# Kernel tuning notes

Measured on AMD Instinct MI355X. Metric: run time of the kernel, lower is better.

The kernel has to match this reference:

```python
import jax, jax.numpy as jnp
import numpy as np

DIM = 256      # channel dim
NW = 7         # n_win per side
HEADS = 8
TOPK = 4
KVW = 4        # kv_per_win (ada_avgpool output side)
EPS = 1e-6


def _dwconv(x, w, b):
    # depthwise conv, NHWC, 'SAME' == padding k//2 for odd kernels
    y = jax.lax.conv_general_dilated(
        x, w, (1, 1), 'SAME',
        dimension_numbers=('NHWC', 'HWIO', 'NHWC'),
        feature_group_count=x.shape[-1])
    return y + b


def _ln(x, g, b):
    mu = x.mean(-1, keepdims=True)
    var = ((x - mu) ** 2).mean(-1, keepdims=True)
    return (x - mu) * jax.lax.rsqrt(var + EPS) * g + b


def _bra(x, qkv_w, qkv_b, wo_w, wo_b, lepe_w, lepe_b):
    # BiLevelRoutingAttention, x: (n, H, W, C)
    n, H, W, C = x.shape
    hw, ww = H // NW, W // NW          # window size (8, 8)
    scale = C ** -0.5                   # qk_dim ** -0.5 (BiFormer uses full qk_dim)
    qkv = x @ qkv_w.T + qkv_b           # (n, H, W, 3C)
    # window partition: n (j hw) (i ww) c -> n (j i) hw ww c
    qkv_win = qkv.reshape(n, NW, hw, NW, ww, 3 * C)
    qkv_win = qkv_win.transpose(0, 1, 3, 2, 4, 5).reshape(n, NW * NW, hw, ww, 3 * C)
    q = qkv_win[..., :C]                # (n, p2, hw, ww, C)
    kv = qkv_win[..., C:]               # (n, p2, hw, ww, 2C)
    # --- window-level routing (q/k detached in torch; no fwd effect) ---
    q_win = q.mean((2, 3))              # (n, p2, C)
    k_win = kv[..., :C].mean((2, 3))    # (n, p2, C)
    logits = jnp.einsum('npc,nqc->npq', q_win * scale, k_win)
    _, idx = jax.lax.top_k(logits, TOPK)            # (n, p2, k)
    # --- kv downsample: adaptive avg pool (hw,ww)->(KVW,KVW), exact 2x2 mean here ---
    fh, fw = hw // KVW, ww // KVW
    kv_pix = kv.reshape(n, NW * NW, KVW, fh, KVW, fw, 2 * C).mean((3, 5))
    kv_pix = kv_pix.reshape(n, NW * NW, KVW * KVW, 2 * C)   # (n, p2, w2, 2C)
    # --- gather top-k windows' kv ---
    kv_sel = jax.vmap(lambda t, ix: t[ix])(kv_pix, idx)     # (n, p2, k, w2, 2C)
    cph = C // HEADS
    k_sel = kv_sel[..., :C].reshape(n, NW * NW, TOPK * KVW * KVW, HEADS, cph)
    v_sel = kv_sel[..., C:].reshape(n, NW * NW, TOPK * KVW * KVW, HEADS, cph)
    q_pix = q.reshape(n, NW * NW, hw * ww, HEADS, cph)
    # --- windowed attention over gathered tokens ---
    att = jnp.einsum('npqmc,npsmc->npmqs', q_pix * scale, k_sel)
    att = jax.nn.softmax(att, axis=-1)
    out = jnp.einsum('npmqs,npsmc->npqmc', att, v_sel)
    out = out.reshape(n, NW, NW, hw, ww, C).transpose(0, 1, 3, 2, 4, 5).reshape(n, H, W, C)
    # --- lepe: depthwise 5x5 on v over the full image ---
    v_img = qkv[..., 2 * C:]
    out = out + _dwconv(v_img, lepe_w, lepe_b)
    return out @ wo_w.T + wo_b


def setup_inputs() -> dict:
    key = jax.random.key(0)
    ks = jax.random.split(key, 8)
    C, s = DIM, 0.02
    p = {}
    p['x'] = jax.random.normal(ks[0], (16, C, 56, 56), jnp.float32)
    p['pos_w'] = jax.random.normal(ks[1], (3, 3, 1, C), jnp.float32) * s
    p['pos_b'] = jnp.zeros((C,), jnp.float32)
    p['ln1_g'] = jnp.ones((C,), jnp.float32)
    p['ln1_b'] = jnp.zeros((C,), jnp.float32)
    p['ln2_g'] = jnp.ones((C,), jnp.float32)
    p['ln2_b'] = jnp.zeros((C,), jnp.float32)
    p['qkv_w'] = jax.random.normal(ks[2], (3 * C, C), jnp.float32) * s
    p['qkv_b'] = jnp.zeros((3 * C,), jnp.float32)
    p['wo_w'] = jax.random.normal(ks[3], (C, C), jnp.float32) * s
    p['wo_b'] = jnp.zeros((C,), jnp.float32)
    p['lepe_w'] = jax.random.normal(ks[4], (5, 5, 1, C), jnp.float32) * s
    p['lepe_b'] = jnp.zeros((C,), jnp.float32)
    p['fc1_w'] = jax.random.normal(ks[5], (4 * C, C), jnp.float32) * s
    p['fc1_b'] = jnp.zeros((4 * C,), jnp.float32)
    p['fc2_w'] = jax.random.normal(ks[6], (C, 4 * C), jnp.float32) * s
    p['fc2_b'] = jnp.zeros((C,), jnp.float32)
    return p


def reference(x, pos_w, pos_b, ln1_g, ln1_b, ln2_g, ln2_b, qkv_w, qkv_b,
              wo_w, wo_b, lepe_w, lepe_b, fc1_w, fc1_b, fc2_w, fc2_b):
    xh = x.transpose(0, 2, 3, 1)                       # NCHW -> NHWC
    xh = xh + _dwconv(xh, pos_w, pos_b)                # pos embed (dw 3x3)
    xh = xh + _bra(_ln(xh, ln1_g, ln1_b), qkv_w, qkv_b, wo_w, wo_b, lepe_w, lepe_b)
    h = _ln(xh, ln2_g, ln2_b)
    h = jax.nn.gelu(h @ fc1_w.T + fc1_b, approximate=False)
    xh = xh + (h @ fc2_w.T + fc2_b)
    return xh.transpose(0, 3, 1, 2)                    # NHWC -> NCHW
```

## Files before the change

kernel.cpp:

```cpp
#include <hip/hip_runtime.h>
#include <math.h>

static constexpr int NIMG = 16;
static constexpr int TOK  = NIMG * 56 * 56;
static constexpr size_t TC = (size_t)TOK * 256;
static constexpr int PTOK = 784 * 16;

typedef __bf16 bf16x8 __attribute__((ext_vector_type(8)));
typedef float  f32x4  __attribute__((ext_vector_type(4)));

__device__ inline float bf2f(unsigned short u) {
  unsigned int i = ((unsigned int)u) << 16; float f; __builtin_memcpy(&f, &i, 4); return f;
}
__device__ inline unsigned short f2bf(float f) {
  unsigned int i; __builtin_memcpy(&i, &f, 4);
  unsigned int r = i + 0x7fffu + ((i >> 16) & 1u);
  return (unsigned short)(r >> 16);
}

__global__ __launch_bounds__(256) void nchw2nhwc(const float* __restrict__ x,
                                                 float* __restrict__ y) {
  __shared__ float T[32][37];
  int nh = blockIdx.z;
  int n = nh / 56, h = nh % 56;
  int c0 = blockIdx.y * 32, w0 = blockIdx.x * 32;
  int tid = threadIdx.x;
  int wlim = 56 - w0; if (wlim > 32) wlim = 32;
  {
    int ci = tid >> 3, w = (tid & 7) * 4;
    if (w < wlim) {
      f32x4 v = *(const f32x4*)&x[(((size_t)n * 256 + c0 + ci) * 56 + h) * 56 + w0 + w];
#pragma unroll
      for (int j = 0; j < 4; j++) T[ci][w + j] = v[j];
    }
  }
  __syncthreads();
  {
    int wi = tid >> 3, cq = tid & 7;
    if (wi < wlim) {
      f32x4 o;
#pragma unroll
      for (int k = 0; k < 4; k++) o[k] = T[cq * 4 + k][wi];
      *(f32x4*)&y[(((size_t)n * 56 + h) * 56 + w0 + wi) * 256 + c0 + cq * 4] = o;
    }
  }
}

__global__ __launch_bounds__(256) void nhwc2nchw(const float* __restrict__ y,
                                                 float* __restrict__ o) {
  __shared__ float T[32][37];
  int nh = blockIdx.z;
  int n = nh / 56, h = nh % 56;
  int w0 = blockIdx.x * 32, c0 = blockIdx.y * 32;
  int tid = threadIdx.x;
  int wlim = 56 - w0; if (wlim > 32) wlim = 32;
  {
    int wi = tid >> 3, cq = tid & 7;
    if (wi < wlim) {
      f32x4 v = *(const f32x4*)&y[(((size_t)n * 56 + h) * 56 + w0 + wi) * 256 + c0 + cq * 4];
#pragma unroll
      for (int k = 0; k < 4; k++) T[wi][cq * 4 + k] = v[k];
    }
  }
  __syncthreads();
  {
    int ci = tid >> 3, w = (tid & 7) * 4;
    if (w < wlim) {
      f32x4 ov;
#pragma unroll
      for (int j = 0; j < 4; j++) ov[j] = T[w + j][ci];
      *(f32x4*)&o[(((size_t)n * 256 + c0 + ci) * 56 + h) * 56 + w0 + w] = ov;
    }
  }
}

__global__ __launch_bounds__(256) void posconv_kernel(const float* __restrict__ xt,
                                                      const float* __restrict__ w,
                                                      const float* __restrict__ b,
                                                      float* __restrict__ xh) {
  int bid = blockIdx.x;
  int wgid = (bid & 7) * 1568 + (bid >> 3);
  int t = wgid * 4 + (threadIdx.x >> 6);
  int lane = threadIdx.x & 63;
  int c = lane * 4;
  int n = t / 3136, rem = t % 3136, h = rem / 56, ww = rem % 56;
  f32x4 acc = *(const f32x4*)&b[c];
  for (int dh = -1; dh <= 1; dh++) {
    int hh = h + dh;
    if ((unsigned)hh >= 56u) continue;
    for (int dw = -1; dw <= 1; dw++) {
      int wc = ww + dw;
      if ((unsigned)wc >= 56u) continue;
      f32x4 xx = *(const f32x4*)&xt[(((size_t)n * 56 + hh) * 56 + wc) * 256 + c];
      f32x4 wv = *(const f32x4*)&w[((dh + 1) * 3 + (dw + 1)) * 256 + c];
      acc += xx * wv;
    }
  }
  f32x4 xv = *(const f32x4*)&xt[(size_t)t * 256 + c];
  *(f32x4*)&xh[(size_t)t * 256 + c] = xv + acc;
}

__global__ __launch_bounds__(256) void lnw_kernel(const float* __restrict__ x,
                                                  const float* __restrict__ g,
                                                  const float* __restrict__ b,
                                                  float* __restrict__ of,
                                                  unsigned short* __restrict__ ob) {
  int t = blockIdx.x * 4 + (threadIdx.x >> 6);
  int lane = threadIdx.x & 63;
  int c = lane * 4;
  f32x4 v = *(const f32x4*)&x[(size_t)t * 256 + c];
  float s = v[0] + v[1] + v[2] + v[3];
#pragma unroll
  for (int m = 1; m < 64; m <<= 1) s += __shfl_xor(s, m);
  float mu = s * (1.f / 256.f);
  f32x4 d = v - mu;
  float ss = d[0] * d[0] + d[1] * d[1] + d[2] * d[2] + d[3] * d[3];
#pragma unroll
  for (int m = 1; m < 64; m <<= 1) ss += __shfl_xor(ss, m);
  float rs = rsqrtf(ss * (1.f / 256.f) + 1e-6f);
  f32x4 gg = *(const f32x4*)&g[c];
  f32x4 bb = *(const f32x4*)&b[c];
  f32x4 y = d * rs * gg + bb;
  if (of) *(f32x4*)&of[(size_t)t * 256 + c] = y;
  if (ob) {
    unsigned short yb[4];
#pragma unroll
    for (int j = 0; j < 4; j++) yb[j] = f2bf(y[j]);
    __builtin_memcpy(ob + (size_t)t * 256 + c, yb, 8);
  }
}

template <bool OUTBF, bool LN2F>
__global__ __launch_bounds__(512, 4) void mgemm2(const unsigned short* __restrict__ A, int lda,
                                                 const unsigned short* __restrict__ B, int ldb,
                                                 const float* __restrict__ bias,
                                                 const float* __restrict__ R,
                                                 void* __restrict__ C_,
                                                 int N, int K, int flags, int gx,
                                                 const float* __restrict__ g2,
                                                 const float* __restrict__ b2,
                                                 unsigned short* __restrict__ ob2) {
  __shared__ unsigned short As[128 * 64];
  __shared__ unsigned short Bs[256 * 64];
  __shared__ float redS[4][128];
  __shared__ float redQ[4][128];
  int tid = threadIdx.x;
  int nwg = gridDim.x, bid = blockIdx.x;
  int q8 = nwg >> 3, r8 = nwg & 7;
  int xcd = bid & 7, pos = bid >> 3;
  int wgid = (xcd < r8 ? xcd * (q8 + 1) : r8 * (q8 + 1) + (xcd - r8) * q8) + pos;
  int m0 = (wgid / gx) * 128;
  int n0 = (wgid % gx) * 256;

  int lane = tid & 63, wid = tid >> 6;
  int wr = (wid >> 2) * 64, wc = (wid & 3) * 64;
  int llo = lane & 15, lhi = lane >> 4;

  f32x4 acc[4][4];
#pragma unroll
  for (int i = 0; i < 4; i++)
#pragma unroll
    for (int j = 0; j < 4; j++) acc[i][j] = (f32x4){0.f, 0.f, 0.f, 0.f};

  for (int k0 = 0; k0 < K; k0 += 64) {
#pragma unroll
    for (int i = 0; i < 2; i++) {
      int qa = tid + 512 * i;
      int row = qa >> 3, col = (qa & 7) ^ (row & 7);
      __builtin_amdgcn_global_load_lds(
          (const __attribute__((address_space(1))) unsigned int*)
              (A + (size_t)(m0 + row) * lda + k0 + col * 8),
          (__attribute__((address_space(3))) unsigned int*)(As + qa * 8), 16, 0, 0);
    }
#pragma unroll
    for (int i = 0; i < 4; i++) {
      int qb = tid + 512 * i;
      int row = qb >> 3, col = (qb & 7) ^ (row & 7);
      __builtin_amdgcn_global_load_lds(
          (const __attribute__((address_space(1))) unsigned int*)
              (B + (size_t)(n0 + row) * ldb + k0 + col * 8),
          (__attribute__((address_space(3))) unsigned int*)(Bs + qb * 8), 16, 0, 0);
    }
    __syncthreads();
#pragma unroll
    for (int ks = 0; ks < 2; ks++) {
      int cchunk = ks * 4 + lhi;
      bf16x8 af[4], bfr[4];
#pragma unroll
      for (int mi = 0; mi < 4; mi++) {
        int r = wr + mi * 16 + llo;
        __builtin_memcpy(&af[mi], As + (size_t)r * 64 + (cchunk ^ (r & 7)) * 8, 16);
      }
#pragma unroll
      for (int nj = 0; nj < 4; nj++) {
        int r = wc + nj * 16 + llo;
        __builtin_memcpy(&bfr[nj], Bs + (size_t)r * 64 + (cchunk ^ (r & 7)) * 8, 16);
      }
#pragma unroll
      for (int mi = 0; mi < 4; mi++)
#pragma unroll
        for (int nj = 0; nj < 4; nj++)
          acc[mi][nj] = __builtin_amdgcn_mfma_f32_16x16x32_bf16(af[mi], bfr[nj],
                                                                acc[mi][nj], 0, 0, 0);
    }
    __syncthreads();
  }

  if constexpr (LN2F) {
    float sr[4][4], qr[4][4];
#pragma unroll
    for (int mi = 0; mi < 4; mi++)
#pragma unroll
      for (int j = 0; j < 4; j++) { sr[mi][j] = 0.f; qr[mi][j] = 0.f; }
#pragma unroll
    for (int mi = 0; mi < 4; mi++)
#pragma unroll
      for (int nj = 0; nj < 4; nj++) {
        int n = wc + nj * 16 + llo;
        float bv = bias[n];
#pragma unroll
        for (int j = 0; j < 4; j++) {
          int m = m0 + wr + mi * 16 + lhi * 4 + j;
          float v = acc[mi][nj][j] + bv + R[(size_t)m * 256 + n];
          acc[mi][nj][j] = v;
          sr[mi][j] += v;
          qr[mi][j] += v * v;
        }
      }
#pragma unroll
    for (int mi = 0; mi < 4; mi++)
#pragma unroll
      for (int j = 0; j < 4; j++)
#pragma unroll
        for (int d = 1; d < 16; d <<= 1) {
          sr[mi][j] += __shfl_xor(sr[mi][j], d);
          qr[mi][j] += __shfl_xor(qr[mi][j], d);
        }
    if (llo == 0) {
#pragma unroll
      for (int mi = 0; mi < 4; mi++)
#pragma unroll
        for (int j = 0; j < 4; j++) {
          int lr = wr + mi * 16 + lhi * 4 + j;
          redS[wid & 3][lr] = sr[mi][j];
          redQ[wid & 3][lr] = qr[mi][j];
        }
    }
    __syncthreads();
#pragma unroll
    for (int mi = 0; mi < 4; mi++)
#pragma unroll
      for (int j = 0; j < 4; j++) {
        int lr = wr + mi * 16 + lhi * 4 + j;
        float S = redS[0][lr] + redS[1][lr] + redS[2][lr] + redS[3][lr];
        float Q = redQ[0][lr] + redQ[1][lr] + redQ[2][lr] + redQ[3][lr];
        float mu = S * (1.f / 256.f);
        float var = Q * (1.f / 256.f) - mu * mu;
        float rs = rsqrtf(var + 1e-6f);
        size_t mrow = (size_t)(m0 + lr) * 256;
#pragma unroll
        for (int nj = 0; nj < 4; nj++) {
          int n = wc + nj * 16 + llo;
          float v = acc[mi][nj][j];
          ((float*)C_)[mrow + n] = v;
          ob2[mrow + n] = f2bf((v - mu) * rs * g2[n] + b2[n]);
        }
      }
  } else {
    int coln = llo, rowg = lhi * 4;
#pragma unroll
    for (int mi = 0; mi < 4; mi++) {
#pragma unroll
      for (int nj = 0; nj < 4; nj++) {
        int n = n0 + wc + nj * 16 + coln;
        float bv = (flags & 8) ? 0.f : bias[n];
#pragma unroll
        for (int j = 0; j < 4; j++) {
          int m = m0 + wr + mi * 16 + rowg + j;
          float v = acc[mi][nj][j] + bv;
          if (flags & 1) v = 0.5f * v * (1.0f + erff(v * 0.70710678118654752f));
          if (flags & 2) v += R[(size_t)m * N + n];
          if (OUTBF) ((unsigned short*)C_)[(size_t)m * N + n] = f2bf(v);
          else       ((float*)C_)[(size_t)m * N + n] = v;
        }
      }
    }
  }
}

__global__ __launch_bounds__(256) void cvt_kernel(const float* __restrict__ s,
                                                  unsigned short* __restrict__ d, int n) {
  int i = blockIdx.x * 256 + threadIdx.x;
  if (i < n) d[i] = f2bf(s[i]);
}

__global__ __launch_bounds__(512) void bqv_kernel(const float* __restrict__ qkv_b,
                                                  float* __restrict__ bqv) {
  int i = threadIdx.x;
  bqv[i] = qkv_b[i < 256 ? i : i + 256];
}

__global__ __launch_bounds__(256) void pool_kernel(const float* __restrict__ x,
                                                   unsigned short* __restrict__ plx,
                                                   float* __restrict__ wmx) {
  int np = blockIdx.x * 4 + (threadIdx.x >> 6);
  int lane = threadIdx.x & 63;
  int c = lane * 4;
  int n = np / 49, p = np % 49, wr = p / 7, wc = p % 7;
  f32x4 tot = (f32x4){0.f, 0.f, 0.f, 0.f};
  for (int s = 0; s < 16; s++) {
    int i = s >> 2, j = s & 3;
    f32x4 a = (f32x4){0.f, 0.f, 0.f, 0.f};
    for (int di = 0; di < 2; di++)
      for (int dj = 0; dj < 2; dj++) {
        size_t t = ((size_t)n * 56 + wr * 8 + i * 2 + di) * 56 + wc * 8 + j * 2 + dj;
        a += *(const f32x4*)&x[t * 256 + c];
      }
    a *= 0.25f;
    unsigned short ab[4];
#pragma unroll
    for (int k = 0; k < 4; k++) ab[k] = f2bf(a[k]);
    __builtin_memcpy(plx + ((size_t)np * 16 + s) * 256 + c, ab, 8);
    tot += a;
  }
  *(f32x4*)&wmx[(size_t)np * 256 + c] = tot * (1.f / 16.f);
}

__global__ __launch_bounds__(256) void winproj_kernel(const float* __restrict__ wmx,
                                                      const float* __restrict__ qkv_w,
                                                      const float* __restrict__ qkv_b,
                                                      float* __restrict__ qkwin) {
  int np = blockIdx.x, t = threadIdx.x;
  __shared__ float xs[256];
  xs[t] = wmx[(size_t)np * 256 + t];
  __syncthreads();
  for (int rep = 0; rep < 2; rep++) {
    int n = t + rep * 256;
    const float* wrow = qkv_w + (size_t)n * 256;
    float s = qkv_b[n];
    for (int c = 0; c < 256; c++) s += xs[c] * wrow[c];
    qkwin[(size_t)np * 512 + n] = s;
  }
}

__global__ __launch_bounds__(64) void topk_kernel(const float* __restrict__ qkwin,
                                                  int* __restrict__ idx) {
  int np = blockIdx.x;
  int n = np / 49;
  int j = threadIdx.x;
  __shared__ float lg[49];
  if (j < 49) {
    const float* qp = qkwin + (size_t)np * 512;
    const float* kp = qkwin + ((size_t)n * 49 + j) * 512 + 256;
    float s = 0.f;
    for (int c = 0; c < 256; c++) s += qp[c] * kp[c];
    lg[j] = s;
  }
  __syncthreads();
  if (j == 0) {
    unsigned long long used = 0ull;
    for (int t = 0; t < 4; t++) {
      float best = -INFINITY;
      int bi = 0;
      for (int q = 0; q < 49; q++)
        if (!((used >> q) & 1ull) && lg[q] > best) { best = lg[q]; bi = q; }
      idx[np * 4 + t] = bi;
      used |= (1ull << bi);
    }
  }
}

__global__ __launch_bounds__(64) void attn_mfma(const unsigned short* __restrict__ qvb,
                                                const unsigned short* __restrict__ kvp,
                                                const int* __restrict__ idx,
                                                unsigned short* __restrict__ out) {
  __shared__ unsigned short Vt[32 * 72];
  __shared__ unsigned short Pl[64 * 72];
  int bid = blockIdx.x;
  int head = bid & 7, np = bid >> 3;
  int n = np / 49, p = np % 49;
  int h0 = (p / 7) * 8, w0 = (p % 7) * 8;
  int lane = threadIdx.x;
  int lhi = lane >> 4, llo = lane & 15;

  int wi4[4];
#pragma unroll
  for (int t = 0; t < 4; t++) wi4[t] = idx[np * 4 + t];

#pragma unroll
  for (int it = 0; it < 4; it++) {
    int cell = lane >> 2;
    int chunk = lane & 3;
    int s = it * 16 + cell;
    const unsigned short* g = kvp + ((size_t)(n * 49 + wi4[it]) * 16 + cell) * 512
                              + 256 + head * 32 + chunk * 8;
    unsigned short vv[8];
    __builtin_memcpy(vv, g, 16);
#pragma unroll
    for (int j = 0; j < 8; j++) Vt[(chunk * 8 + j) * 72 + s] = vv[j];
  }

  bf16x8 qf[4], kf[4];
#pragma unroll
  for (int mi = 0; mi < 4; mi++) {
    int row = mi * 16 + llo;
    int h = h0 + (row >> 3), w = w0 + (row & 7);
    __builtin_memcpy(&qf[mi],
                     qvb + (((size_t)n * 56 + h) * 56 + w) * 512 + head * 32 + lhi * 8, 16);
  }
#pragma unroll
  for (int nj = 0; nj < 4; nj++) {
    __builtin_memcpy(&kf[nj],
                     kvp + ((size_t)(n * 49 + wi4[nj]) * 16 + llo) * 512 + head * 32 + lhi * 8,
                     16);
  }

  f32x4 acc[4][4];
#pragma unroll
  for (int mi = 0; mi < 4; mi++)
#pragma unroll
    for (int nj = 0; nj < 4; nj++) acc[mi][nj] = (f32x4){0.f, 0.f, 0.f, 0.f};
#pragma unroll
  for (int mi = 0; mi < 4; mi++)
#pragma unroll
    for (int nj = 0; nj < 4; nj++)
      acc[mi][nj] = __builtin_amdgcn_mfma_f32_16x16x32_bf16(qf[mi], kf[nj], acc[mi][nj], 0, 0, 0);

#pragma unroll
  for (int mi = 0; mi < 4; mi++)
#pragma unroll
    for (int nj = 0; nj < 4; nj++) acc[mi][nj] *= 0.0625f;
#pragma unroll
  for (int mi = 0; mi < 4; mi++) {
#pragma unroll
    for (int reg = 0; reg < 4; reg++) {
      float m = fmaxf(fmaxf(acc[mi][0][reg], acc[mi][1][reg]),
                      fmaxf(acc[mi][2][reg], acc[mi][3][reg]));
      m = fmaxf(m, __shfl_xor(m, 1));
      m = fmaxf(m, __shfl_xor(m, 2));
      m = fmaxf(m, __shfl_xor(m, 4));
      m = fmaxf(m, __shfl_xor(m, 8));
      float sum = 0.f;
#pragma unroll
      for (int nj = 0; nj < 4; nj++) {
        float e = __expf(acc[mi][nj][reg] - m);
        acc[mi][nj][reg] = e;
        sum += e;
      }
      sum += __shfl_xor(sum, 1);
      sum += __shfl_xor(sum, 2);
      sum += __shfl_xor(sum, 4);
      sum += __shfl_xor(sum, 8);
      float inv = 1.0f / sum;
#pragma unroll
      for (int nj = 0; nj < 4; nj++) acc[mi][nj][reg] *= inv;
    }
  }

#pragma unroll
  for (int mi = 0; mi < 4; mi++)
#pragma unroll
    for (int nj = 0; nj < 4; nj++)
#pragma unroll
      for (int reg = 0; reg < 4; reg++) {
        int row = mi * 16 + lhi * 4 + reg;
        Pl[row * 72 + nj * 16 + llo] = f2bf(acc[mi][nj][reg]);
      }

  f32x4 o[4][2];
#pragma unroll
  for (int mi = 0; mi < 4; mi++)
#pragma unroll
    for (int nc = 0; nc < 2; nc++) o[mi][nc] = (f32x4){0.f, 0.f, 0.f, 0.f};
#pragma unroll
  for (int ks = 0; ks < 2; ks++) {
    bf16x8 pa[4], vb[2];
#pragma unroll
    for (int mi = 0; mi < 4; mi++)
      __builtin_memcpy(&pa[mi], Pl + (mi * 16 + llo) * 72 + ks * 32 + lhi * 8, 16);
#pragma unroll
    for (int nc = 0; nc < 2; nc++)
      __builtin_memcpy(&vb[nc], Vt + (nc * 16 + llo) * 72 + ks * 32 + lhi * 8, 16);
#pragma unroll
    for (int mi = 0; mi < 4; mi++)
#pragma unroll
      for (int nc = 0; nc < 2; nc++)
        o[mi][nc] = __builtin_amdgcn_mfma_f32_16x16x32_bf16(pa[mi], vb[nc], o[mi][nc], 0, 0, 0);
  }

#pragma unroll
  for (int mi = 0; mi < 4; mi++)
#pragma unroll
    for (int nc = 0; nc < 2; nc++)
#pragma unroll
      for (int reg = 0; reg < 4; reg++) {
        int row = mi * 16 + lhi * 4 + reg;
        int h = h0 + (row >> 3), w = w0 + (row & 7);
        out[(((size_t)n * 56 + h) * 56 + w) * 256 + head * 32 + nc * 16 + llo] =
            f2bf(o[mi][nc][reg]);
      }
}

__global__ __launch_bounds__(256) void lepe_kernel(const unsigned short* __restrict__ qvb,
                                                   const float* __restrict__ w,
                                                   const float* __restrict__ b,
                                                   unsigned short* __restrict__ out) {
  int bid = blockIdx.x;
  int wgid = (bid & 7) * 784 + (bid >> 3);
  int t = wgid * 8 + (threadIdx.x >> 5);
  int cg = threadIdx.x & 31;
  int c = cg * 8;
  int n = t / 3136, rem = t % 3136, h = rem / 56, ww = rem % 56;
  float acc[8];
#pragma unroll
  for (int j = 0; j < 8; j++) acc[j] = b[c + j];
  for (int dh = -2; dh <= 2; dh++) {
    int hh = h + dh;
    if ((unsigned)hh >= 56u) continue;
    for (int dw = -2; dw <= 2; dw++) {
      int wc = ww + dw;
      if ((unsigned)wc >= 56u) continue;
      unsigned short vv[8];
      __builtin_memcpy(vv, qvb + (((size_t)n * 56 + hh) * 56 + wc) * 512 + 256 + c, 16);
      const float* wp = w + ((dh + 2) * 5 + (dw + 2)) * 256 + c;
#pragma unroll
      for (int j = 0; j < 8; j++) acc[j] += bf2f(vv[j]) * wp[j];
    }
  }
  size_t o = (size_t)t * 256 + c;
  unsigned short ov[8];
  __builtin_memcpy(ov, out + o, 16);
#pragma unroll
  for (int j = 0; j < 8; j++) ov[j] = f2bf(bf2f(ov[j]) + acc[j]);
  __builtin_memcpy(out + o, ov, 16);
}

extern "C" void kernel_launch(void* const* d_in, const int* in_sizes, int n_in,
                              void* d_out, int out_size, void* d_ws, size_t ws_size,
                              hipStream_t stream) {
  const float* x      = (const float*)d_in[0];
  const float* pos_w  = (const float*)d_in[1];
  const float* pos_b  = (const float*)d_in[2];
  const float* ln1_g  = (const float*)d_in[3];
  const float* ln1_b  = (const float*)d_in[4];
  const float* ln2_g  = (const float*)d_in[5];
  const float* ln2_b  = (const float*)d_in[6];
  const float* qkv_w  = (const float*)d_in[7];
  const float* qkv_b  = (const float*)d_in[8];
  const float* wo_w   = (const float*)d_in[9];
  const float* wo_b   = (const float*)d_in[10];
  const float* lepe_w = (const float*)d_in[11];
  const float* lepe_b = (const float*)d_in[12];
  const float* fc1_w  = (const float*)d_in[13];
  const float* fc1_b  = (const float*)d_in[14];
  const float* fc2_w  = (const float*)d_in[15];
  const float* fc2_b  = (const float*)d_in[16];

  float*          xt   = (float*)d_out;
  float*          lnf  = (float*)d_out;
  unsigned short* qvb  = (unsigned short*)d_out;
  unsigned short* hbuf = (unsigned short*)d_out;

  float*          r2   = (float*)d_ws;
  float*          wmx  = r2 + TC;
  float*          qkw  = wmx + (size_t)784 * 256;
  float*          bqv  = qkw + (size_t)784 * 512;
  unsigned short* lnb  = (unsigned short*)(bqv + 512);
  unsigned short* aob  = lnb;
  unsigned short* ln2b = lnb;
  unsigned short* plx  = lnb + TC;
  unsigned short* kvp  = plx + (size_t)PTOK * 256;
  unsigned short* wqv  = kvp + (size_t)PTOK * 512;
  unsigned short* wkv  = wqv + (size_t)512 * 256;
  unsigned short* wwo  = wkv + (size_t)512 * 256;
  unsigned short* wfc1 = wwo + (size_t)256 * 256;
  unsigned short* wfc2 = wfc1 + (size_t)1024 * 256;
  int*            idx  = (int*)(wfc2 + (size_t)256 * 1024);

  cvt_kernel<<<(65536 + 255) / 256, 256, 0, stream>>>(qkv_w, wqv, 65536);
  cvt_kernel<<<(65536 + 255) / 256, 256, 0, stream>>>(qkv_w + (size_t)512 * 256, wqv + 65536, 65536);
  cvt_kernel<<<(131072 + 255) / 256, 256, 0, stream>>>(qkv_w + (size_t)256 * 256, wkv, 131072);
  cvt_kernel<<<(65536 + 255) / 256, 256, 0, stream>>>(wo_w, wwo, 65536);
  cvt_kernel<<<(262144 + 255) / 256, 256, 0, stream>>>(fc1_w, wfc1, 262144);
  cvt_kernel<<<(262144 + 255) / 256, 256, 0, stream>>>(fc2_w, wfc2, 262144);
  bqv_kernel<<<1, 512, 0, stream>>>(qkv_b, bqv);

  dim3 tb(32, 8);
  nchw2nhwc<<<dim3(2, 8, NIMG * 56), 256, 0, stream>>>(x, xt);
  posconv_kernel<<<TOK / 4, 256, 0, stream>>>(xt, pos_w, pos_b, r2);
  lnw_kernel<<<TOK / 4, 256, 0, stream>>>(r2, ln1_g, ln1_b, lnf, lnb);
  pool_kernel<<<196, 256, 0, stream>>>(lnf, plx, wmx);
  mgemm2<true, false><<<784, 512, 0, stream>>>(lnb, 256, wqv, 256, bqv, nullptr,
                                               qvb, 512, 256, 0, 2,
                                               nullptr, nullptr, nullptr);
  mgemm2<true, false><<<196, 512, 0, stream>>>(plx, 256, wkv, 256, qkv_b + 256, nullptr,
                                               kvp, 512, 256, 0, 2,
                                               nullptr, nullptr, nullptr);
  winproj_kernel<<<784, 256, 0, stream>>>(wmx, qkv_w, qkv_b, qkw);
  topk_kernel<<<784, 64, 0, stream>>>(qkw, idx);
  attn_mfma<<<6272, 64, 0, stream>>>(qvb, kvp, idx, aob);
  lepe_kernel<<<TOK / 8, 256, 0, stream>>>(qvb, lepe_w, lepe_b, aob);
  mgemm2<false, true><<<392, 512, 0, stream>>>(aob, 256, wwo, 256, wo_b, r2,
                                               r2, 256, 256, 2, 1,
                                               ln2_g, ln2_b, ln2b);
  mgemm2<true, false><<<784, 512, 0, stream>>>(ln2b, 256, wfc1, 256, fc1_b, nullptr,
                                               hbuf, 512, 256, 1, 2,
                                               nullptr, nullptr, nullptr);
  mgemm2<false, false><<<392, 512, 0, stream>>>(hbuf, 512, wfc2, 1024, fc2_b, r2,
                                                r2, 256, 512, 2, 1,
                                                nullptr, nullptr, nullptr);
  mgemm2<true, false><<<784, 512, 0, stream>>>(ln2b, 256, wfc1 + (size_t)512 * 256, 256,
                                               fc1_b + 512, nullptr,
                                               hbuf, 512, 256, 1, 2,
                                               nullptr, nullptr, nullptr);
  mgemm2<false, false><<<392, 512, 0, stream>>>(hbuf, 512, wfc2 + 512, 1024, fc2_b, r2,
                                                r2, 256, 512, 2 | 8, 1,
                                                nullptr, nullptr, nullptr);
  nhwc2nchw<<<dim3(2, 8, NIMG * 56), 256, 0, stream>>>(r2, (float*)d_out);
}
```

Before: 508.1 us.

## Fuse pos-conv with LN1, merge weight conversions, branchless conv loads

Merges the depthwise positional conv and LayerNorm1 into one kernel that writes the residual, the bf16 LN output, and per-token mean/rstd. This drops the fp32 LN output buffer and its round trip. The pool kernel now rebuilds the normalized values from the residual plus the stored stats. The seven weight-conversion and bias launches become one prep kernel. Both the pos conv and the lepe conv now issue all neighbor loads up front with clamped indices and masks instead of branching, which raises register pressure in the lepe kernel.

Result: faster. 479.5 us (-5.6%).

```diff
diff --git a/kernel.cpp b/kernel.cpp
--- a/kernel.cpp
+++ b/kernel.cpp
@@ -74,41 +74,41 @@
   }
 }
 
-__global__ __launch_bounds__(256) void posconv_kernel(const float* __restrict__ xt,
-                                                      const float* __restrict__ w,
-                                                      const float* __restrict__ b,
-                                                      float* __restrict__ xh) {
+__global__ __launch_bounds__(256) void posln_kernel(const float* __restrict__ xt,
+                                                    const float* __restrict__ w,
+                                                    const float* __restrict__ bb,
+                                                    const float* __restrict__ g1,
+                                                    const float* __restrict__ b1,
+                                                    float* __restrict__ xh,
+                                                    unsigned short* __restrict__ lnb,
+                                                    float* __restrict__ murs) {
   int bid = blockIdx.x;
   int wgid = (bid & 7) * 1568 + (bid >> 3);
   int t = wgid * 4 + (threadIdx.x >> 6);
   int lane = threadIdx.x & 63;
   int c = lane * 4;
   int n = t / 3136, rem = t % 3136, h = rem / 56, ww = rem % 56;
-  f32x4 acc = *(const f32x4*)&b[c];
-  for (int dh = -1; dh <= 1; dh++) {
-    int hh = h + dh;
-    if ((unsigned)hh >= 56u) continue;
-    for (int dw = -1; dw <= 1; dw++) {
-      int wc = ww + dw;
-      if ((unsigned)wc >= 56u) continue;
-      f32x4 xx = *(const f32x4*)&xt[(((size_t)n * 56 + hh) * 56 + wc) * 256 + c];
-      f32x4 wv = *(const f32x4*)&w[((dh + 1) * 3 + (dw + 1)) * 256 + c];
-      acc += xx * wv;
-    }
-  }
-  f32x4 xv = *(const f32x4*)&xt[(size_t)t * 256 + c];
-  *(f32x4*)&xh[(size_t)t * 256 + c] = xv + acc;
-}
-
-__global__ __launch_bounds__(256) void lnw_kernel(const float* __restrict__ x,
-                                                  const float* __restrict__ g,
-                                                  const float* __restrict__ b,
-                                                  float* __restrict__ of,
-                                                  unsigned short* __restrict__ ob) {
-  int t = blockIdx.x * 4 + (threadIdx.x >> 6);
-  int lane = threadIdx.x & 63;
-  int c = lane * 4;
-  f32x4 v = *(const f32x4*)&x[(size_t)t * 256 + c];
+  const float* base = xt + (size_t)n * 3136 * 256 + c;
+
+  f32x4 xx[9]; float msk[9];
+#pragma unroll
+  for (int k = 0; k < 9; k++) {
+    int dh = k / 3 - 1, dw = k % 3 - 1;
+    int hh = h + dh, wc = ww + dw;
+    msk[k] = ((unsigned)hh < 56u && (unsigned)wc < 56u) ? 1.f : 0.f;
+    int hcl = hh < 0 ? 0 : (hh > 55 ? 55 : hh);
+    int wcl = wc < 0 ? 0 : (wc > 55 ? 55 : wc);
+    xx[k] = *(const f32x4*)&base[(size_t)(hcl * 56 + wcl) * 256];
+  }
+  f32x4 acc = *(const f32x4*)&bb[c];
+#pragma unroll
+  for (int k = 0; k < 9; k++) {
+    f32x4 wv = *(const f32x4*)&w[k * 256 + c];
+    acc += xx[k] * (wv * msk[k]);
+  }
+  f32x4 v = xx[4] + acc;
+  *(f32x4*)&xh[(size_t)t * 256 + c] = v;
+
   float s = v[0] + v[1] + v[2] + v[3];
 #pragma unroll
   for (int m = 1; m < 64; m <<= 1) s += __shfl_xor(s, m);
@@ -118,15 +118,16 @@
 #pragma unroll
   for (int m = 1; m < 64; m <<= 1) ss += __shfl_xor(ss, m);
   float rs = rsqrtf(ss * (1.f / 256.f) + 1e-6f);
-  f32x4 gg = *(const f32x4*)&g[c];
-  f32x4 bb = *(const f32x4*)&b[c];
-  f32x4 y = d * rs * gg + bb;
-  if (of) *(f32x4*)&of[(size_t)t * 256 + c] = y;
-  if (ob) {
-    unsigned short yb[4];
-#pragma unroll
-    for (int j = 0; j < 4; j++) yb[j] = f2bf(y[j]);
-    __builtin_memcpy(ob + (size_t)t * 256 + c, yb, 8);
+  f32x4 gg = *(const f32x4*)&g1[c];
+  f32x4 b4 = *(const f32x4*)&b1[c];
+  f32x4 y = d * rs * gg + b4;
+  unsigned short yb[4];
+#pragma unroll
+  for (int j = 0; j < 4; j++) yb[j] = f2bf(y[j]);
+  __builtin_memcpy(lnb + (size_t)t * 256 + c, yb, 8);
+  if (lane == 0) {
+    murs[2 * (size_t)t] = mu;
+    murs[2 * (size_t)t + 1] = rs;
   }
 }
 
@@ -288,42 +289,60 @@
   }
 }
 
-__global__ __launch_bounds__(256) void cvt_kernel(const float* __restrict__ s,
-                                                  unsigned short* __restrict__ d, int n) {
+__global__ __launch_bounds__(256) void prep_kernel(const float* __restrict__ qkv_w,
+                                                   const float* __restrict__ qkv_b,
+                                                   const float* __restrict__ wo_w,
+                                                   const float* __restrict__ fc1_w,
+                                                   const float* __restrict__ fc2_w,
+                                                   unsigned short* __restrict__ wqv,
+                                                   unsigned short* __restrict__ wkv,
+                                                   unsigned short* __restrict__ wwo,
+                                                   unsigned short* __restrict__ wfc1,
+                                                   unsigned short* __restrict__ wfc2,
+                                                   float* __restrict__ bqv) {
   int i = blockIdx.x * 256 + threadIdx.x;
-  if (i < n) d[i] = f2bf(s[i]);
-}
-
-__global__ __launch_bounds__(512) void bqv_kernel(const float* __restrict__ qkv_b,
-                                                  float* __restrict__ bqv) {
-  int i = threadIdx.x;
-  bqv[i] = qkv_b[i < 256 ? i : i + 256];
-}
-
-__global__ __launch_bounds__(256) void pool_kernel(const float* __restrict__ x,
+  if (i < 65536) { wqv[i] = f2bf(qkv_w[i]); }
+  else if (i < 131072) { int j = i - 65536; wqv[65536 + j] = f2bf(qkv_w[512 * 256 + j]); }
+  else if (i < 262144) { int j = i - 131072; wkv[j] = f2bf(qkv_w[256 * 256 + j]); }
+  else if (i < 327680) { int j = i - 262144; wwo[j] = f2bf(wo_w[j]); }
+  else if (i < 589824) { int j = i - 327680; wfc1[j] = f2bf(fc1_w[j]); }
+  else if (i < 851968) { int j = i - 589824; wfc2[j] = f2bf(fc2_w[j]); }
+  else if (i < 852480) { int j = i - 851968; bqv[j] = qkv_b[j < 256 ? j : j + 256]; }
+}
+
+__global__ __launch_bounds__(256) void pool_kernel(const float* __restrict__ xh,
+                                                   const float* __restrict__ murs,
+                                                   const float* __restrict__ g1,
+                                                   const float* __restrict__ b1,
                                                    unsigned short* __restrict__ plx,
                                                    float* __restrict__ wmx) {
   int np = blockIdx.x * 4 + (threadIdx.x >> 6);
   int lane = threadIdx.x & 63;
   int c = lane * 4;
-  int n = np / 49, p = np % 49, wr = p / 7, wc = p % 7;
+  int n = np / 49, p = np % 49, wr = p / 7, wcq = p % 7;
+  f32x4 g4 = *(const f32x4*)&g1[c];
+  f32x4 b4 = *(const f32x4*)&b1[c];
   f32x4 tot = (f32x4){0.f, 0.f, 0.f, 0.f};
   for (int s = 0; s < 16; s++) {
     int i = s >> 2, j = s & 3;
-    f32x4 a = (f32x4){0.f, 0.f, 0.f, 0.f};
+    f32x4 z = (f32x4){0.f, 0.f, 0.f, 0.f};
     for (int di = 0; di < 2; di++)
       for (int dj = 0; dj < 2; dj++) {
-        size_t t = ((size_t)n * 56 + wr * 8 + i * 2 + di) * 56 + wc * 8 + j * 2 + dj;
-        a += *(const f32x4*)&x[t * 256 + c];
-      }
-    a *= 0.25f;
+        size_t t = ((size_t)n * 56 + wr * 8 + i * 2 + di) * 56 + wcq * 8 + j * 2 + dj;
+        float mu = murs[2 * t], rs = murs[2 * t + 1];
+        f32x4 v = *(const f32x4*)&xh[t * 256 + c];
+        z += (v - mu) * rs;
+      }
+    z *= 0.25f;
+    f32x4 cell = z * g4 + b4;
     unsigned short ab[4];
 #pragma unroll
-    for (int k = 0; k < 4; k++) ab[k] = f2bf(a[k]);
+    for (int k = 0; k < 4; k++) ab[k] = f2bf(cell[k]);
     __builtin_memcpy(plx + ((size_t)np * 16 + s) * 256 + c, ab, 8);
-    tot += a;
-  }
-  *(f32x4*)&wmx[(size_t)np * 256 + c] = tot * (1.f / 16.f);
+    tot += z;
+  }
+  f32x4 wm = tot * (1.f / 16.f) * g4 + b4;
+  *(f32x4*)&wmx[(size_t)np * 256 + c] = wm;
 }
 
 __global__ __launch_bounds__(256) void winproj_kernel(const float* __restrict__ wmx,
@@ -511,22 +530,30 @@
   int cg = threadIdx.x & 31;
   int c = cg * 8;
   int n = t / 3136, rem = t % 3136, h = rem / 56, ww = rem % 56;
+  const unsigned short* vbase = qvb + (size_t)n * 3136 * 512 + 256 + c;
+
+  unsigned short vv[25][8];
+  float msk[25];
+#pragma unroll
+  for (int k = 0; k < 25; k++) {
+    int dh = k / 5 - 2, dw = k % 5 - 2;
+    int hh = h + dh, wc = ww + dw;
+    msk[k] = ((unsigned)hh < 56u && (unsigned)wc < 56u) ? 1.f : 0.f;
+    int hcl = hh < 0 ? 0 : (hh > 55 ? 55 : hh);
+    int wcl = wc < 0 ? 0 : (wc > 55 ? 55 : wc);
+    __builtin_memcpy(&vv[k][0], vbase + (size_t)(hcl * 56 + wcl) * 512, 16);
+  }
+
   float acc[8];
 #pragma unroll
   for (int j = 0; j < 8; j++) acc[j] = b[c + j];
-  for (int dh = -2; dh <= 2; dh++) {
-    int hh = h + dh;
-    if ((unsigned)hh >= 56u) continue;
-    for (int dw = -2; dw <= 2; dw++) {
-      int wc = ww + dw;
-      if ((unsigned)wc >= 56u) continue;
-      unsigned short vv[8];
-      __builtin_memcpy(vv, qvb + (((size_t)n * 56 + hh) * 56 + wc) * 512 + 256 + c, 16);
-      const float* wp = w + ((dh + 2) * 5 + (dw + 2)) * 256 + c;
-#pragma unroll
-      for (int j = 0; j < 8; j++) acc[j] += bf2f(vv[j]) * wp[j];
-    }
-  }
+#pragma unroll
+  for (int k = 0; k < 25; k++) {
+    const float* wp = w + k * 256 + c;
+#pragma unroll
+    for (int j = 0; j < 8; j++) acc[j] += bf2f(vv[k][j]) * (wp[j] * msk[k]);
+  }
+
   size_t o = (size_t)t * 256 + c;
   unsigned short ov[8];
   __builtin_memcpy(ov, out + o, 16);
@@ -557,7 +584,6 @@
   const float* fc2_b  = (const float*)d_in[16];
 
   float*          xt   = (float*)d_out;
-  float*          lnf  = (float*)d_out;
   unsigned short* qvb  = (unsigned short*)d_out;
   unsigned short* hbuf = (unsigned short*)d_out;
 
@@ -576,20 +602,14 @@
   unsigned short* wfc1 = wwo + (size_t)256 * 256;
   unsigned short* wfc2 = wfc1 + (size_t)1024 * 256;
   int*            idx  = (int*)(wfc2 + (size_t)256 * 1024);
-
-  cvt_kernel<<<(65536 + 255) / 256, 256, 0, stream>>>(qkv_w, wqv, 65536);
-  cvt_kernel<<<(65536 + 255) / 256, 256, 0, stream>>>(qkv_w + (size_t)512 * 256, wqv + 65536, 65536);
-  cvt_kernel<<<(131072 + 255) / 256, 256, 0, stream>>>(qkv_w + (size_t)256 * 256, wkv, 131072);
-  cvt_kernel<<<(65536 + 255) / 256, 256, 0, stream>>>(wo_w, wwo, 65536);
-  cvt_kernel<<<(262144 + 255) / 256, 256, 0, stream>>>(fc1_w, wfc1, 262144);
-  cvt_kernel<<<(262144 + 255) / 256, 256, 0, stream>>>(fc2_w, wfc2, 262144);
-  bqv_kernel<<<1, 512, 0, stream>>>(qkv_b, bqv);
-
-  dim3 tb(32, 8);
+  float*          murs = (float*)(idx + 784 * 4);
+
+  prep_kernel<<<3330, 256, 0, stream>>>(qkv_w, qkv_b, wo_w, fc1_w, fc2_w,
+                                        wqv, wkv, wwo, wfc1, wfc2, bqv);
   nchw2nhwc<<<dim3(2, 8, NIMG * 56), 256, 0, stream>>>(x, xt);
-  posconv_kernel<<<TOK / 4, 256, 0, stream>>>(xt, pos_w, pos_b, r2);
-  lnw_kernel<<<TOK / 4, 256, 0, stream>>>(r2, ln1_g, ln1_b, lnf, lnb);
-  pool_kernel<<<196, 256, 0, stream>>>(lnf, plx, wmx);
+  posln_kernel<<<TOK / 4, 256, 0, stream>>>(xt, pos_w, pos_b, ln1_g, ln1_b,
+                                            r2, lnb, murs);
+  pool_kernel<<<196, 256, 0, stream>>>(r2, murs, ln1_g, ln1_b, plx, wmx);
   mgemm2<true, false><<<784, 512, 0, stream>>>(lnb, 256, wqv, 256, bqv, nullptr,
                                                qvb, 512, 256, 0, 2,
                                                nullptr, nullptr, nullptr);
```
